# Optimization experiments

Hardware: AMD Instinct MI355X
Metric: run time of the kernel (lower is better)

## Reference

```python
import jax, jax.numpy as jnp
import numpy as np

B, C, H, W = 8, 64, 128, 128


def _conv3x3(x, w, b):
    # x: [B,C,H,W], w: [O,I,3,3], b: [O]; stride 1, padding 1
    y = jax.lax.conv_general_dilated(
        x, w, window_strides=(1, 1), padding=((1, 1), (1, 1)),
        dimension_numbers=('NCHW', 'OIHW', 'NCHW'))
    return y + b[None, :, None, None]


def setup_inputs() -> dict:
    key = jax.random.key(0)
    ks = jax.random.split(key, 8)
    s = 0.05
    return {
        'x': jax.random.normal(ks[0], (B, C, H, W), jnp.float32),
        'Wq': jax.random.normal(ks[1], (C, C, 3, 3), jnp.float32) * s,
        'bq': jax.random.normal(ks[2], (C,), jnp.float32) * s,
        'Wk': jax.random.normal(ks[3], (C, C, 3, 3), jnp.float32) * s,
        'bk': jax.random.normal(ks[4], (C,), jnp.float32) * s,
        'Wv': jax.random.normal(ks[5], (C, C, 3, 3), jnp.float32) * s,
        'bv': jax.random.normal(ks[6], (C,), jnp.float32) * s,
        'gamma': jax.random.normal(ks[7], (1,), jnp.float32) * s,
    }


def reference(x, Wq, bq, Wk, bk, Wv, bv, gamma):
    b_, c_, h_, w_ = x.shape
    q = _conv3x3(x, Wq, bq)  # [B,C,H,W]
    k = _conv3x3(x, Wk, bk)
    v = _conv3x3(x, Wv, bv)

    # energy along H (column attention): eH[b,h,w,g] = sum_c q[b,c,h,w]*k[b,c,g,w]
    eH = jnp.einsum('bchw,bcgw->bhwg', q, k)
    eye = jnp.eye(h_, dtype=bool)  # mask diagonal h==g with -inf
    eH = jnp.where(eye[None, :, None, :], -jnp.inf, eH)

    # energy along W (row attention): eW[b,h,w,g] = sum_c q[b,c,h,w]*k[b,c,h,g]
    eW = jnp.einsum('bchw,bchg->bhwg', q, k)

    # joint softmax over concatenated [H | W] axis
    att = jax.nn.softmax(jnp.concatenate([eH, eW], axis=3), axis=3)
    att_H = att[:, :, :, :h_]          # [B,H,W,H]
    att_W = att[:, :, :, h_:h_ + w_]   # [B,H,W,W]

    out_H = jnp.einsum('bcgw,bhwg->bchw', v, att_H)
    out_W = jnp.einsum('bchg,bhwg->bchw', v, att_W)

    return gamma[0] * (out_H + out_W) + x
```

## Files before the change

kernel.cpp:

```cpp
#include <hip/hip_runtime.h>
#include <hip/hip_bf16.h>

#define B_ 8
#define C_ 64
#define H_ 128
#define W_ 128
#define HW_  ((size_t)H_ * W_)
#define CHW_ ((size_t)C_ * H_ * W_)

typedef unsigned short u16;
typedef unsigned int   u32;
typedef __attribute__((ext_vector_type(8))) short bf16x8;
typedef __attribute__((ext_vector_type(4))) float f32x4;

__device__ __forceinline__ float bf2f(u16 h) {
    union { u32 u; float f; } c; c.u = ((u32)h) << 16; return c.f;
}
__device__ __forceinline__ u16 f2bf(float f) {
    union { float f; u32 u; } c; c.f = f;
    u32 u = c.u;
    u32 r = (u + 0x7fffu + ((u >> 16) & 1u)) >> 16;
    return (u16)r;
}
__device__ __forceinline__ u32 pack2(float a, float b) {
    return (u32)f2bf(a) | ((u32)f2bf(b) << 16);
}
__device__ __forceinline__ float sanit(float x, float lo, float hi) {
    return fminf(fmaxf(x, lo), hi);
}
__device__ __forceinline__ void gload_lds16(const u16* g, u16* l) {
    __builtin_amdgcn_global_load_lds(
        (const __attribute__((address_space(1))) void*)g,
        (__attribute__((address_space(3))) void*)l, 16, 0, 0);
}

__global__ __launch_bounds__(256) void prep_weights(
    const float* __restrict__ Wq, const float* __restrict__ Wk,
    const float* __restrict__ Wv, u16* __restrict__ Wt)
{
    int tap = blockIdx.x;
    int cog = blockIdx.y * 4 + (threadIdx.x >> 6);
    int ci  = threadIdx.x & 63;
    int arr = cog >> 6, co = cog & 63;
    const float* src = arr == 0 ? Wq : (arr == 1 ? Wk : Wv);
    Wt[tap * 12288 + cog * 64 + ci] = f2bf(src[(co * 64 + ci) * 9 + tap]);
}

__global__ __launch_bounds__(256) void xprep_kernel(
    const float* __restrict__ x, u16* __restrict__ xb)
{
    const int hp  = blockIdx.x;
    const int tid = threadIdx.x;
    u16* dst = xb + ((size_t)blockIdx.y * 130 + hp) * 8192;
    if (hp == 0 || hp == 129) {
#pragma unroll
        for (int i = 0; i < 4; i++)
            *(uint4*)(dst + (size_t)(tid + i * 256) * 8) = (uint4){0, 0, 0, 0};
        return;
    }
    const float* xr = x + (size_t)blockIdx.y * CHW_ + (size_t)(hp - 1) * W_;
#pragma unroll
    for (int it = 0; it < 4; it++) {
        int idx = tid + it * 256;
        int px  = idx & 127;
        int g   = idx >> 7;
        float vb[8];
#pragma unroll
        for (int e = 0; e < 8; e++)
            vb[e] = xr[(size_t)(g * 8 + e) * HW_ + px];
        uint4 o;
        o.x = pack2(vb[0], vb[1]);
        o.y = pack2(vb[2], vb[3]);
        o.z = pack2(vb[4], vb[5]);
        o.w = pack2(vb[6], vb[7]);
        *(uint4*)(dst + (size_t)(g * 128 + px) * 8) = o;
    }
}

__global__ __launch_bounds__(256, 2) void conv_mfma_kernel(
    const u16* __restrict__ xb, const u16* __restrict__ Wt,
    const float* __restrict__ bq, const float* __restrict__ bk,
    const float* __restrict__ bv,
    u16* __restrict__ qN, u16* __restrict__ kN, u16* __restrict__ v)
{
    const int nwg  = gridDim.x * gridDim.y;
    const int flat = blockIdx.y * gridDim.x + blockIdx.x;
    const int wg   = (flat & 7) * (nwg >> 3) + (flat >> 3);
    const int h    = wg & (H_ - 1);
    const int bidx = wg >> 7;
    const size_t boff = (size_t)bidx * CHW_;
    const int tid  = threadIdx.x;
    const int lane = tid & 63, wv = tid >> 6;
    const int ln15 = lane & 15, quad = lane >> 4;

    __shared__ __align__(16) u16 xI[24960];

    const int woff = (wv * 16 + ln15) * 64 + quad * 8;

    bf16x8 wcur[2][3], wnxt[2][3];
#pragma unroll
    for (int ks = 0; ks < 2; ks++)
#pragma unroll
        for (int mt = 0; mt < 3; mt++)
            wcur[ks][mt] = *(const bf16x8*)(Wt + woff + mt * 4096 + ks * 32);

    if (tid < 48) {
        int dh = tid >> 4, g = (tid & 15) >> 1, p = (tid & 1) ? 129 : 0;
        *(uint4*)(xI + dh * 8320 + g * 1040 + p * 8) = (uint4){0, 0, 0, 0};
    }

    const u16* xrows = xb + ((size_t)bidx * 130 + h) * 8192;
#pragma unroll
    for (int it = 0; it < 12; it++) {
        int chunk = wv * 12 + it;
        int dh = chunk >> 4, g = (chunk >> 1) & 7, half = chunk & 1;
        gload_lds16(xrows + (size_t)dh * 8192 + g * 1024 + half * 512 + lane * 8,
                    xI + dh * 8320 + g * 1040 + 8 + half * 512);
    }
    __syncthreads();

    f32x4 acc[3][8];
#pragma unroll
    for (int mt = 0; mt < 3; mt++)
#pragma unroll
        for (int nt = 0; nt < 8; nt++)
            acc[mt][nt] = (f32x4){0.f, 0.f, 0.f, 0.f};

#pragma unroll
    for (int tap = 0; tap < 9; tap++) {
        const int dh = tap / 3, dw = tap % 3;
        if (tap < 8) {
#pragma unroll
            for (int ks = 0; ks < 2; ks++)
#pragma unroll
                for (int mt = 0; mt < 3; mt++)
                    wnxt[ks][mt] = *(const bf16x8*)(Wt + (tap + 1) * 12288 + woff + mt * 4096 + ks * 32);
        }
        const u16* xrow = xI + dh * 8320;
#pragma unroll
        for (int ks = 0; ks < 2; ks++) {
            bf16x8 bfr[8];
#pragma unroll
            for (int nt = 0; nt < 8; nt++)
                bfr[nt] = *(const bf16x8*)(xrow + ((quad + ks * 4) * 1040 + (nt * 16 + ln15 + dw) * 8));
            __builtin_amdgcn_s_setprio(1);
#pragma unroll
            for (int mt = 0; mt < 3; mt++)
#pragma unroll
                for (int nt = 0; nt < 8; nt++)
                    acc[mt][nt] = __builtin_amdgcn_mfma_f32_16x16x32_bf16(
                        wcur[ks][mt], bfr[nt], acc[mt][nt], 0, 0, 0);
            __builtin_amdgcn_s_setprio(0);
        }
        if (tap < 8) {
#pragma unroll
            for (int ks = 0; ks < 2; ks++)
#pragma unroll
                for (int mt = 0; mt < 3; mt++)
                    wcur[ks][mt] = wnxt[ks][mt];
        }
    }

    const int cb = wv * 16 + quad * 4;
#pragma unroll
    for (int mt = 0; mt < 3; mt++) {
        const float* bias = mt == 0 ? bq : (mt == 1 ? bk : bv);
        float b0 = bias[cb], b1 = bias[cb + 1], b2 = bias[cb + 2], b3 = bias[cb + 3];
        if (mt < 2) {
            u16* dst = (mt ? kN : qN) + boff + (size_t)h * W_ * 64 + cb;
#pragma unroll
            for (int nt = 0; nt < 8; nt++) {
                int px = nt * 16 + ln15;
                u32 p0 = pack2(acc[mt][nt][0] + b0, acc[mt][nt][1] + b1);
                u32 p1 = pack2(acc[mt][nt][2] + b2, acc[mt][nt][3] + b3);
                *(u32*)(dst + (size_t)px * 64)     = p0;
                *(u32*)(dst + (size_t)px * 64 + 2) = p1;
            }
        } else {
            float bb[4] = {b0, b1, b2, b3};
#pragma unroll
            for (int r = 0; r < 4; r++) {
                u16* drow = v + boff + (size_t)(cb + r) * HW_ + (size_t)h * W_;
#pragma unroll
                for (int nt = 0; nt < 8; nt++)
                    drow[nt * 16 + ln15] = f2bf(acc[mt][nt][r] + bb[r]);
            }
        }
    }
}

__global__ __launch_bounds__(256) void vt_kernel(
    const u16* __restrict__ v, u16* __restrict__ vT)
{
    __shared__ u16 Ts[64 * 72];
    const u16* src = v  + (size_t)blockIdx.z * CHW_ + (size_t)blockIdx.y * HW_;
    u16* dst       = vT + (size_t)blockIdx.z * CHW_ + (size_t)blockIdx.y * HW_;
    const int ti = blockIdx.x & 1, tj = blockIdx.x >> 1;
    const int r0 = ti * 64, c0 = tj * 64;
    const int tid = threadIdx.x;
    const int r = tid >> 2, cq = tid & 3;
#pragma unroll
    for (int i = 0; i < 2; i++) {
        uint4 u = *(const uint4*)(src + (size_t)(r0 + r) * 128 + c0 + cq * 16 + i * 8);
        *(uint4*)(Ts + r * 72 + cq * 16 + i * 8) = u;
    }
    __syncthreads();
    const int wr = tid >> 2, hq = tid & 3;
    union { u16 o[16]; uint4 v4[2]; } t;
#pragma unroll
    for (int j = 0; j < 16; j++) t.o[j] = Ts[(hq * 16 + j) * 72 + wr];
    *(uint4*)(dst + (size_t)(c0 + wr) * 128 + r0 + hq * 16)     = t.v4[0];
    *(uint4*)(dst + (size_t)(c0 + wr) * 128 + r0 + hq * 16 + 8) = t.v4[1];
}

__global__ __launch_bounds__(256, 3) void col_kernel(
    const u16* __restrict__ qN, const u16* __restrict__ kN,
    const u16* __restrict__ vT,
    float* __restrict__ maxH, float* __restrict__ sumH,
    float* __restrict__ Ocol)
{
    const size_t boff = (size_t)blockIdx.z * CHW_;
    const size_t soff = (size_t)blockIdx.z * HW_;
    qN += boff; kN += boff; vT += boff; Ocol += boff;
    maxH += soff; sumH += soff;

    const int s    = blockIdx.x;
    const int tid  = threadIdx.x;
    const int lane = tid & 63, wv = tid >> 6;
    const int ln15 = lane & 15, quad = lane >> 4;

    __shared__ __align__(16) u16 smemU[18432];
    u16* Qs = smemU;
    u16* Ks = smemU + 9216;

#pragma unroll
    for (int it = 0; it < 4; it++) {
        int idx = tid + it * 256;
        int t = idx >> 3, cg = (idx & 7) * 8;
        size_t off = (size_t)t * 8192 + (size_t)s * 64 + cg;
        *(uint4*)(Qs + t * 72 + cg) = *(const uint4*)(qN + off);
        *(uint4*)(Ks + t * 72 + cg) = *(const uint4*)(kN + off);
    }
    __syncthreads();

    f32x4 Sc[2][8];
#pragma unroll
    for (int mt = 0; mt < 2; mt++)
#pragma unroll
        for (int nt = 0; nt < 8; nt++)
            Sc[mt][nt] = (f32x4){0.f, 0.f, 0.f, 0.f};

#pragma unroll
    for (int ks = 0; ks < 2; ks++) {
        bf16x8 aq[2];
#pragma unroll
        for (int mt = 0; mt < 2; mt++)
            aq[mt] = *(const bf16x8*)(Qs + (wv * 32 + mt * 16 + ln15) * 72 + ks * 32 + quad * 8);
#pragma unroll
        for (int nt = 0; nt < 8; nt++) {
            bf16x8 bk_ = *(const bf16x8*)(Ks + (nt * 16 + ln15) * 72 + ks * 32 + quad * 8);
#pragma unroll
            for (int mt = 0; mt < 2; mt++)
                Sc[mt][nt] = __builtin_amdgcn_mfma_f32_16x16x32_bf16(aq[mt], bk_, Sc[mt][nt], 0, 0, 0);
        }
    }
#pragma unroll
    for (int mt = 0; mt < 2; mt++)
#pragma unroll
        for (int nt = 0; nt < 8; nt++)
#pragma unroll
            for (int r = 0; r < 4; r++) {
                int tt = wv * 32 + mt * 16 + quad * 4 + r;
                if (tt == nt * 16 + ln15) Sc[mt][nt][r] = -1e30f;
            }

#pragma unroll
    for (int mt = 0; mt < 2; mt++)
#pragma unroll
        for (int r = 0; r < 4; r++) {
            float m = Sc[mt][0][r];
#pragma unroll
            for (int nt = 1; nt < 8; nt++) m = fmaxf(m, Sc[mt][nt][r]);
            for (int o = 1; o < 16; o <<= 1) m = fmaxf(m, __shfl_xor(m, o));
            float ss = 0.f;
#pragma unroll
            for (int nt = 0; nt < 8; nt++) {
                float e = __expf(Sc[mt][nt][r] - m);
                ss += e;
                Sc[mt][nt][r] = e;
            }
            for (int o = 1; o < 16; o <<= 1) ss += __shfl_xor(ss, o);
            if (ln15 == 0) {
                int tt = wv * 32 + mt * 16 + quad * 4 + r;
                int pix = tt * W_ + s;
                maxH[pix] = m; sumH[pix] = ss;
            }
        }
    __syncthreads();
    u16* Ps = smemU;
#pragma unroll
    for (int mt = 0; mt < 2; mt++)
#pragma unroll
        for (int nt = 0; nt < 8; nt++)
#pragma unroll
            for (int r = 0; r < 4; r++)
                Ps[(wv * 32 + mt * 16 + quad * 4 + r) * 136 + nt * 16 + ln15] =
                    f2bf(Sc[mt][nt][r]);
    __syncthreads();

    f32x4 Oc[2][4];
#pragma unroll
    for (int mt = 0; mt < 2; mt++)
#pragma unroll
        for (int nt = 0; nt < 4; nt++)
            Oc[mt][nt] = (f32x4){0.f, 0.f, 0.f, 0.f};
#pragma unroll
    for (int kg = 0; kg < 4; kg++) {
        bf16x8 ap[2];
#pragma unroll
        for (int mt = 0; mt < 2; mt++)
            ap[mt] = *(const bf16x8*)(Ps + (wv * 32 + mt * 16 + ln15) * 136 + kg * 32 + quad * 8);
#pragma unroll
        for (int nt = 0; nt < 4; nt++) {
            bf16x8 bv_ = *(const bf16x8*)(vT + (size_t)(nt * 16 + ln15) * HW_ + (size_t)s * 128 + kg * 32 + quad * 8);
#pragma unroll
            for (int mt = 0; mt < 2; mt++)
                Oc[mt][nt] = __builtin_amdgcn_mfma_f32_16x16x32_bf16(ap[mt], bv_, Oc[mt][nt], 0, 0, 0);
        }
    }
    __syncthreads();
    float* Of = (float*)smemU;
#pragma unroll
    for (int mt = 0; mt < 2; mt++)
#pragma unroll
        for (int nt = 0; nt < 4; nt++)
#pragma unroll
            for (int r = 0; r < 4; r++)
                Of[(wv * 32 + mt * 16 + quad * 4 + r) * 68 + nt * 16 + ln15] = Oc[mt][nt][r];
    __syncthreads();
#pragma unroll
    for (int it = 0; it < 8; it++) {
        int idx = tid + it * 256;
        int t = idx >> 4, c4 = (idx & 15) * 4;
        *(float4*)(Ocol + ((size_t)t * 128 + s) * 64 + c4) = *(float4*)(Of + t * 68 + c4);
    }
}

__global__ __launch_bounds__(256, 3) void row_kernel(
    const u16* __restrict__ qN, const u16* __restrict__ kN,
    const u16* __restrict__ v,
    const float* __restrict__ x, const float* __restrict__ gammap,
    const float* __restrict__ maxH, const float* __restrict__ sumH,
    const float* __restrict__ Ocol, float* __restrict__ out)
{
    const size_t boff = (size_t)blockIdx.z * CHW_;
    const size_t soff = (size_t)blockIdx.z * HW_;
    qN += boff; kN += boff; v += boff; Ocol += boff; x += boff; out += boff;
    maxH += soff; sumH += soff;

    const int s    = blockIdx.x;
    const int tid  = threadIdx.x;
    const int lane = tid & 63, wv = tid >> 6;
    const int ln15 = lane & 15, quad = lane >> 4;

    __shared__ __align__(16) u16 smemU[18432];
    u16* Qs = smemU;
    u16* Ks = smemU + 9216;

    float mcv[2][4], scv[2][4];
#pragma unroll
    for (int mt = 0; mt < 2; mt++)
#pragma unroll
        for (int r = 0; r < 4; r++) {
            int tt = wv * 32 + mt * 16 + quad * 4 + r;
            mcv[mt][r] = maxH[s * W_ + tt];
            scv[mt][r] = sumH[s * W_ + tt];
        }

#pragma unroll
    for (int it = 0; it < 4; it++) {
        int idx = tid + it * 256;
        int t = idx >> 3, cg = (idx & 7) * 8;
        size_t off = (size_t)s * 8192 + (size_t)t * 64 + cg;
        *(uint4*)(Qs + t * 72 + cg) = *(const uint4*)(qN + off);
        *(uint4*)(Ks + t * 72 + cg) = *(const uint4*)(kN + off);
    }
    __syncthreads();

    f32x4 Sc[2][8];
#pragma unroll
    for (int mt = 0; mt < 2; mt++)
#pragma unroll
        for (int nt = 0; nt < 8; nt++)
            Sc[mt][nt] = (f32x4){0.f, 0.f, 0.f, 0.f};
#pragma unroll
    for (int ks = 0; ks < 2; ks++) {
        bf16x8 aq[2];
#pragma unroll
        for (int mt = 0; mt < 2; mt++)
            aq[mt] = *(const bf16x8*)(Qs + (wv * 32 + mt * 16 + ln15) * 72 + ks * 32 + quad * 8);
#pragma unroll
        for (int nt = 0; nt < 8; nt++) {
            bf16x8 bk_ = *(const bf16x8*)(Ks + (nt * 16 + ln15) * 72 + ks * 32 + quad * 8);
#pragma unroll
            for (int mt = 0; mt < 2; mt++)
                Sc[mt][nt] = __builtin_amdgcn_mfma_f32_16x16x32_bf16(aq[mt], bk_, Sc[mt][nt], 0, 0, 0);
        }
    }

    float be[2][4], al[2][4];
#pragma unroll
    for (int mt = 0; mt < 2; mt++)
#pragma unroll
        for (int r = 0; r < 4; r++) {
            float m = Sc[mt][0][r];
#pragma unroll
            for (int nt = 1; nt < 8; nt++) m = fmaxf(m, Sc[mt][nt][r]);
            for (int o = 1; o < 16; o <<= 1) m = fmaxf(m, __shfl_xor(m, o));
            float ss = 0.f;
#pragma unroll
            for (int nt = 0; nt < 8; nt++) {
                float e = __expf(Sc[mt][nt][r] - m);
                ss += e;
                Sc[mt][nt][r] = e;
            }
            for (int o = 1; o < 16; o <<= 1) ss += __shfl_xor(ss, o);
            float mc = sanit(mcv[mt][r], -3e38f, 3e38f);
            float sc = sanit(scv[mt][r], 0.f, 3e38f);
            float mm = fmaxf(mc, m);
            float dd = sc * __expf(fminf(mc - mm, 0.f)) + ss * __expf(m - mm);
            float rv = 1.0f / fmaxf(dd, 1e-30f);
            be[mt][r] = __expf(m - mm) * rv;
            al[mt][r] = __expf(fminf(mc - mm, 0.f)) * rv;
        }
    __syncthreads();
    u16* Ps = smemU;
#pragma unroll
    for (int mt = 0; mt < 2; mt++)
#pragma unroll
        for (int nt = 0; nt < 8; nt++)
#pragma unroll
            for (int r = 0; r < 4; r++)
                Ps[(wv * 32 + mt * 16 + quad * 4 + r) * 136 + nt * 16 + ln15] =
                    f2bf(Sc[mt][nt][r] * be[mt][r]);
    __syncthreads();

    f32x4 Oc[2][4];
#pragma unroll
    for (int mt = 0; mt < 2; mt++)
#pragma unroll
        for (int nt = 0; nt < 4; nt++)
            Oc[mt][nt] = (f32x4){0.f, 0.f, 0.f, 0.f};
#pragma unroll
    for (int kg = 0; kg < 4; kg++) {
        bf16x8 ap[2];
#pragma unroll
        for (int mt = 0; mt < 2; mt++)
            ap[mt] = *(const bf16x8*)(Ps + (wv * 32 + mt * 16 + ln15) * 136 + kg * 32 + quad * 8);
#pragma unroll
        for (int nt = 0; nt < 4; nt++) {
            bf16x8 bv_ = *(const bf16x8*)(v + (size_t)(nt * 16 + ln15) * HW_ + (size_t)s * 128 + kg * 32 + quad * 8);
#pragma unroll
            for (int mt = 0; mt < 2; mt++)
                Oc[mt][nt] = __builtin_amdgcn_mfma_f32_16x16x32_bf16(ap[mt], bv_, Oc[mt][nt], 0, 0, 0);
        }
    }
    __syncthreads();

    const float gmm = gammap[0];
    float* Of = (float*)smemU;
#pragma unroll
    for (int mt = 0; mt < 2; mt++)
#pragma unroll
        for (int nt = 0; nt < 4; nt++) {
            float fv[4];
            int c = nt * 16 + ln15;
#pragma unroll
            for (int r = 0; r < 4; r++) {
                int tt = wv * 32 + mt * 16 + quad * 4 + r;
                float oc = Ocol[((size_t)s * 128 + tt) * 64 + c];
                fv[r] = gmm * (Oc[mt][nt][r] + al[mt][r] * oc);
            }
            int w0 = wv * 32 + mt * 16 + quad * 4;
            *(float4*)(Of + c * 132 + w0) = make_float4(fv[0], fv[1], fv[2], fv[3]);
        }
    __syncthreads();
    int c = tid >> 2, w0 = (tid & 3) * 32;
#pragma unroll
    for (int i = 0; i < 8; i++) {
        int w = w0 + i * 4;
        float4 xo = *(const float4*)(x + (size_t)c * HW_ + (size_t)s * 128 + w);
        float4 of = *(const float4*)(Of + c * 132 + w);
        *(float4*)(out + (size_t)c * HW_ + (size_t)s * 128 + w) =
            make_float4(of.x + xo.x, of.y + xo.y, of.z + xo.z, of.w + xo.w);
    }
}

extern "C" void kernel_launch(void* const* d_in, const int* in_sizes, int n_in,
                              void* d_out, int out_size, void* d_ws, size_t ws_size,
                              hipStream_t stream)
{
    const float* x  = (const float*)d_in[0];
    const float* Wq = (const float*)d_in[1];
    const float* bq = (const float*)d_in[2];
    const float* Wk = (const float*)d_in[3];
    const float* bk = (const float*)d_in[4];
    const float* Wv = (const float*)d_in[5];
    const float* bv = (const float*)d_in[6];
    const float* gm = (const float*)d_in[7];
    float* out = (float*)d_out;

    char* ws = (char*)d_ws;
    const size_t need1 = 4 * (size_t)B_ * CHW_ * 2 + (size_t)B_ * CHW_ * 4
                       + 2 * (size_t)B_ * HW_ * 4 + 221184;
    int passes = (ws_size >= need1) ? 1 : 2;
    int nb = B_ / passes;

    const size_t SL = (size_t)nb * CHW_ * 2;
    const size_t OC = (size_t)nb * CHW_ * 4;
    const size_t ST = (size_t)nb * HW_ * 4;
    u16*   qNb  = (u16*)(ws);
    u16*   kNb  = (u16*)(ws + SL);
    u16*   v    = (u16*)(ws + 2 * SL);
    u16*   vT   = (u16*)(ws + 3 * SL);
    float* Ocol = (float*)(ws + 4 * SL);
    float* maxH = (float*)(ws + 4 * SL + OC);
    float* sumH = (float*)(ws + 4 * SL + OC + ST);
    u16*   Wt   = (u16*)(ws + 4 * SL + OC + 2 * ST);
    u16*   xb   = (u16*)Ocol;

    dim3 blk(256);
    prep_weights<<<dim3(9, 48), blk, 0, stream>>>(Wq, Wk, Wv, Wt);

    for (int p = 0; p < passes; p++) {
        const float* xbp = x + (size_t)p * nb * CHW_;
        float* ob = out + (size_t)p * nb * CHW_;
        xprep_kernel<<<dim3(130, nb), blk, 0, stream>>>(xbp, xb);
        conv_mfma_kernel<<<dim3(H_, nb), blk, 0, stream>>>(xb, Wt, bq, bk, bv, qNb, kNb, v);
        vt_kernel<<<dim3(4, C_, nb), blk, 0, stream>>>(v, vT);
        col_kernel<<<dim3(W_, 1, nb), blk, 0, stream>>>(qNb, kNb, vT, maxH, sumH, Ocol);
        row_kernel<<<dim3(H_, 1, nb), blk, 0, stream>>>(qNb, kNb, v, xbp, gm, maxH, sumH, Ocol, ob);
    }
}
```

Baseline: 198.5 us.

## Split conv pixel tiles across blocks and use 512-thread attention blocks

The conv kernel now launches a z-dimension of 2, so each block computes half of a row's pixels with fewer accumulators, and its occupancy hint rises to 3. The col and row attention kernels go from 256 to 512 threads, so each wave handles 16 query rows instead of 32. The goal is more parallelism and lower register pressure on these small grids. In exchange, each conv block still stages the full input rows and weights, so that traffic is duplicated, and per-wave reuse of the loaded K/V fragments drops.

```diff
diff --git a/kernel.cpp b/kernel.cpp
--- a/kernel.cpp
+++ b/kernel.cpp
@@ -77,7 +77,7 @@
     }
 }
 
-__global__ __launch_bounds__(256, 2) void conv_mfma_kernel(
+__global__ __launch_bounds__(256, 3) void conv_mfma_kernel(
     const u16* __restrict__ xb, const u16* __restrict__ Wt,
     const float* __restrict__ bq, const float* __restrict__ bk,
     const float* __restrict__ bv,
@@ -88,6 +88,7 @@
     const int wg   = (flat & 7) * (nwg >> 3) + (flat >> 3);
     const int h    = wg & (H_ - 1);
     const int bidx = wg >> 7;
+    const int p    = blockIdx.z;
     const size_t boff = (size_t)bidx * CHW_;
     const int tid  = threadIdx.x;
     const int lane = tid & 63, wv = tid >> 6;
@@ -105,8 +106,8 @@
             wcur[ks][mt] = *(const bf16x8*)(Wt + woff + mt * 4096 + ks * 32);
 
     if (tid < 48) {
-        int dh = tid >> 4, g = (tid & 15) >> 1, p = (tid & 1) ? 129 : 0;
-        *(uint4*)(xI + dh * 8320 + g * 1040 + p * 8) = (uint4){0, 0, 0, 0};
+        int dh = tid >> 4, g = (tid & 15) >> 1, pp = (tid & 1) ? 129 : 0;
+        *(uint4*)(xI + dh * 8320 + g * 1040 + pp * 8) = (uint4){0, 0, 0, 0};
     }
 
     const u16* xrows = xb + ((size_t)bidx * 130 + h) * 8192;
@@ -119,13 +120,14 @@
     }
     __syncthreads();
 
-    f32x4 acc[3][8];
+    f32x4 acc[3][4];
 #pragma unroll
     for (int mt = 0; mt < 3; mt++)
 #pragma unroll
-        for (int nt = 0; nt < 8; nt++)
+        for (int nt = 0; nt < 4; nt++)
             acc[mt][nt] = (f32x4){0.f, 0.f, 0.f, 0.f};
 
+    const int pxb = p * 64;
 #pragma unroll
     for (int tap = 0; tap < 9; tap++) {
         const int dh = tap / 3, dw = tap % 3;
@@ -139,15 +141,15 @@
         const u16* xrow = xI + dh * 8320;
 #pragma unroll
         for (int ks = 0; ks < 2; ks++) {
-            bf16x8 bfr[8];
-#pragma unroll
-            for (int nt = 0; nt < 8; nt++)
-                bfr[nt] = *(const bf16x8*)(xrow + ((quad + ks * 4) * 1040 + (nt * 16 + ln15 + dw) * 8));
+            bf16x8 bfr[4];
+#pragma unroll
+            for (int nt = 0; nt < 4; nt++)
+                bfr[nt] = *(const bf16x8*)(xrow + ((quad + ks * 4) * 1040 + (pxb + nt * 16 + ln15 + dw) * 8));
             __builtin_amdgcn_s_setprio(1);
 #pragma unroll
             for (int mt = 0; mt < 3; mt++)
 #pragma unroll
-                for (int nt = 0; nt < 8; nt++)
+                for (int nt = 0; nt < 4; nt++)
                     acc[mt][nt] = __builtin_amdgcn_mfma_f32_16x16x32_bf16(
                         wcur[ks][mt], bfr[nt], acc[mt][nt], 0, 0, 0);
             __builtin_amdgcn_s_setprio(0);
@@ -169,8 +171,8 @@
         if (mt < 2) {
             u16* dst = (mt ? kN : qN) + boff + (size_t)h * W_ * 64 + cb;
 #pragma unroll
-            for (int nt = 0; nt < 8; nt++) {
-                int px = nt * 16 + ln15;
+            for (int nt = 0; nt < 4; nt++) {
+                int px = pxb + nt * 16 + ln15;
                 u32 p0 = pack2(acc[mt][nt][0] + b0, acc[mt][nt][1] + b1);
                 u32 p1 = pack2(acc[mt][nt][2] + b2, acc[mt][nt][3] + b3);
                 *(u32*)(dst + (size_t)px * 64)     = p0;
@@ -182,8 +184,8 @@
             for (int r = 0; r < 4; r++) {
                 u16* drow = v + boff + (size_t)(cb + r) * HW_ + (size_t)h * W_;
 #pragma unroll
-                for (int nt = 0; nt < 8; nt++)
-                    drow[nt * 16 + ln15] = f2bf(acc[mt][nt][r] + bb[r]);
+                for (int nt = 0; nt < 4; nt++)
+                    drow[pxb + nt * 16 + ln15] = f2bf(acc[mt][nt][r] + bb[r]);
             }
         }
     }
@@ -213,7 +215,7 @@
     *(uint4*)(dst + (size_t)(c0 + wr) * 128 + r0 + hq * 16 + 8) = t.v4[1];
 }
 
-__global__ __launch_bounds__(256, 3) void col_kernel(
+__global__ __launch_bounds__(512, 4) void col_kernel(
     const u16* __restrict__ qN, const u16* __restrict__ kN,
     const u16* __restrict__ vT,
     float* __restrict__ maxH, float* __restrict__ sumH,
@@ -234,8 +236,8 @@
     u16* Ks = smemU + 9216;
 
 #pragma unroll
-    for (int it = 0; it < 4; it++) {
-        int idx = tid + it * 256;
+    for (int it = 0; it < 2; it++) {
+        int idx = tid + it * 512;
         int t = idx >> 3, cg = (idx & 7) * 8;
         size_t off = (size_t)t * 8192 + (size_t)s * 64 + cg;
         *(uint4*)(Qs + t * 72 + cg) = *(const uint4*)(qN + off);
@@ -243,110 +245,87 @@
     }
     __syncthreads();
 
-    f32x4 Sc[2][8];
-#pragma unroll
-    for (int mt = 0; mt < 2; mt++)
-#pragma unroll
-        for (int nt = 0; nt < 8; nt++)
-            Sc[mt][nt] = (f32x4){0.f, 0.f, 0.f, 0.f};
+    f32x4 Sc[8];
+#pragma unroll
+    for (int nt = 0; nt < 8; nt++)
+        Sc[nt] = (f32x4){0.f, 0.f, 0.f, 0.f};
 
 #pragma unroll
     for (int ks = 0; ks < 2; ks++) {
-        bf16x8 aq[2];
-#pragma unroll
-        for (int mt = 0; mt < 2; mt++)
-            aq[mt] = *(const bf16x8*)(Qs + (wv * 32 + mt * 16 + ln15) * 72 + ks * 32 + quad * 8);
+        bf16x8 aq = *(const bf16x8*)(Qs + (wv * 16 + ln15) * 72 + ks * 32 + quad * 8);
 #pragma unroll
         for (int nt = 0; nt < 8; nt++) {
             bf16x8 bk_ = *(const bf16x8*)(Ks + (nt * 16 + ln15) * 72 + ks * 32 + quad * 8);
-#pragma unroll
-            for (int mt = 0; mt < 2; mt++)
-                Sc[mt][nt] = __builtin_amdgcn_mfma_f32_16x16x32_bf16(aq[mt], bk_, Sc[mt][nt], 0, 0, 0);
-        }
-    }
-#pragma unroll
-    for (int mt = 0; mt < 2; mt++)
-#pragma unroll
-        for (int nt = 0; nt < 8; nt++)
-#pragma unroll
-            for (int r = 0; r < 4; r++) {
-                int tt = wv * 32 + mt * 16 + quad * 4 + r;
-                if (tt == nt * 16 + ln15) Sc[mt][nt][r] = -1e30f;
-            }
-
-#pragma unroll
-    for (int mt = 0; mt < 2; mt++)
+            Sc[nt] = __builtin_amdgcn_mfma_f32_16x16x32_bf16(aq, bk_, Sc[nt], 0, 0, 0);
+        }
+    }
+#pragma unroll
+    for (int nt = 0; nt < 8; nt++)
 #pragma unroll
         for (int r = 0; r < 4; r++) {
-            float m = Sc[mt][0][r];
-#pragma unroll
-            for (int nt = 1; nt < 8; nt++) m = fmaxf(m, Sc[mt][nt][r]);
-            for (int o = 1; o < 16; o <<= 1) m = fmaxf(m, __shfl_xor(m, o));
-            float ss = 0.f;
-#pragma unroll
-            for (int nt = 0; nt < 8; nt++) {
-                float e = __expf(Sc[mt][nt][r] - m);
-                ss += e;
-                Sc[mt][nt][r] = e;
-            }
-            for (int o = 1; o < 16; o <<= 1) ss += __shfl_xor(ss, o);
-            if (ln15 == 0) {
-                int tt = wv * 32 + mt * 16 + quad * 4 + r;
-                int pix = tt * W_ + s;
-                maxH[pix] = m; sumH[pix] = ss;
-            }
-        }
+            int tt = wv * 16 + quad * 4 + r;
+            if (tt == nt * 16 + ln15) Sc[nt][r] = -1e30f;
+        }
+
+#pragma unroll
+    for (int r = 0; r < 4; r++) {
+        float m = Sc[0][r];
+#pragma unroll
+        for (int nt = 1; nt < 8; nt++) m = fmaxf(m, Sc[nt][r]);
+        for (int o = 1; o < 16; o <<= 1) m = fmaxf(m, __shfl_xor(m, o));
+        float ss = 0.f;
+#pragma unroll
+        for (int nt = 0; nt < 8; nt++) {
+            float e = __expf(Sc[nt][r] - m);
+            ss += e;
+            Sc[nt][r] = e;
+        }
+        for (int o = 1; o < 16; o <<= 1) ss += __shfl_xor(ss, o);
+        if (ln15 == 0) {
+            int tt = wv * 16 + quad * 4 + r;
+            int pix = tt * W_ + s;
+            maxH[pix] = m; sumH[pix] = ss;
+        }
+    }
     __syncthreads();
     u16* Ps = smemU;
 #pragma unroll
-    for (int mt = 0; mt < 2; mt++)
-#pragma unroll
-        for (int nt = 0; nt < 8; nt++)
-#pragma unroll
-            for (int r = 0; r < 4; r++)
-                Ps[(wv * 32 + mt * 16 + quad * 4 + r) * 136 + nt * 16 + ln15] =
-                    f2bf(Sc[mt][nt][r]);
-    __syncthreads();
-
-    f32x4 Oc[2][4];
-#pragma unroll
-    for (int mt = 0; mt < 2; mt++)
-#pragma unroll
-        for (int nt = 0; nt < 4; nt++)
-            Oc[mt][nt] = (f32x4){0.f, 0.f, 0.f, 0.f};
+    for (int nt = 0; nt < 8; nt++)
+#pragma unroll
+        for (int r = 0; r < 4; r++)
+            Ps[(wv * 16 + quad * 4 + r) * 136 + nt * 16 + ln15] = f2bf(Sc[nt][r]);
+    __syncthreads();
+
+    f32x4 Oc[4];
+#pragma unroll
+    for (int nt = 0; nt < 4; nt++)
+        Oc[nt] = (f32x4){0.f, 0.f, 0.f, 0.f};
 #pragma unroll
     for (int kg = 0; kg < 4; kg++) {
-        bf16x8 ap[2];
-#pragma unroll
-        for (int mt = 0; mt < 2; mt++)
-            ap[mt] = *(const bf16x8*)(Ps + (wv * 32 + mt * 16 + ln15) * 136 + kg * 32 + quad * 8);
+        bf16x8 ap = *(const bf16x8*)(Ps + (wv * 16 + ln15) * 136 + kg * 32 + quad * 8);
 #pragma unroll
         for (int nt = 0; nt < 4; nt++) {
             bf16x8 bv_ = *(const bf16x8*)(vT + (size_t)(nt * 16 + ln15) * HW_ + (size_t)s * 128 + kg * 32 + quad * 8);
-#pragma unroll
-            for (int mt = 0; mt < 2; mt++)
-                Oc[mt][nt] = __builtin_amdgcn_mfma_f32_16x16x32_bf16(ap[mt], bv_, Oc[mt][nt], 0, 0, 0);
+            Oc[nt] = __builtin_amdgcn_mfma_f32_16x16x32_bf16(ap, bv_, Oc[nt], 0, 0, 0);
         }
     }
     __syncthreads();
     float* Of = (float*)smemU;
 #pragma unroll
-    for (int mt = 0; mt < 2; mt++)
-#pragma unroll
-        for (int nt = 0; nt < 4; nt++)
-#pragma unroll
-            for (int r = 0; r < 4; r++)
-                Of[(wv * 32 + mt * 16 + quad * 4 + r) * 68 + nt * 16 + ln15] = Oc[mt][nt][r];
-    __syncthreads();
-#pragma unroll
-    for (int it = 0; it < 8; it++) {
-        int idx = tid + it * 256;
+    for (int nt = 0; nt < 4; nt++)
+#pragma unroll
+        for (int r = 0; r < 4; r++)
+            Of[(wv * 16 + quad * 4 + r) * 68 + nt * 16 + ln15] = Oc[nt][r];
+    __syncthreads();
+#pragma unroll
+    for (int it = 0; it < 4; it++) {
+        int idx = tid + it * 512;
         int t = idx >> 4, c4 = (idx & 15) * 4;
         *(float4*)(Ocol + ((size_t)t * 128 + s) * 64 + c4) = *(float4*)(Of + t * 68 + c4);
     }
 }
 
-__global__ __launch_bounds__(256, 3) void row_kernel(
+__global__ __launch_bounds__(512, 4) void row_kernel(
     const u16* __restrict__ qN, const u16* __restrict__ kN,
     const u16* __restrict__ v,
     const float* __restrict__ x, const float* __restrict__ gammap,
@@ -367,19 +346,17 @@
     u16* Qs = smemU;
     u16* Ks = smemU + 9216;
 
-    float mcv[2][4], scv[2][4];
-#pragma unroll
-    for (int mt = 0; mt < 2; mt++)
-#pragma unroll
-        for (int r = 0; r < 4; r++) {
-            int tt = wv * 32 + mt * 16 + quad * 4 + r;
-            mcv[mt][r] = maxH[s * W_ + tt];
-            scv[mt][r] = sumH[s * W_ + tt];
-        }
-
-#pragma unroll
-    for (int it = 0; it < 4; it++) {
-        int idx = tid + it * 256;
+    float mcv[4], scv[4];
+#pragma unroll
+    for (int r = 0; r < 4; r++) {
+        int tt = wv * 16 + quad * 4 + r;
+        mcv[r] = maxH[s * W_ + tt];
+        scv[r] = sumH[s * W_ + tt];
+    }
+
+#pragma unroll
+    for (int it = 0; it < 2; it++) {
+        int idx = tid + it * 512;
         int t = idx >> 3, cg = (idx & 7) * 8;
         size_t off = (size_t)s * 8192 + (size_t)t * 64 + cg;
         *(uint4*)(Qs + t * 72 + cg) = *(const uint4*)(qN + off);
@@ -387,82 +364,64 @@
     }
     __syncthreads();
 
-    f32x4 Sc[2][8];
-#pragma unroll
-    for (int mt = 0; mt < 2; mt++)
-#pragma unroll
-        for (int nt = 0; nt < 8; nt++)
-            Sc[mt][nt] = (f32x4){0.f, 0.f, 0.f, 0.f};
+    f32x4 Sc[8];
+#pragma unroll
+    for (int nt = 0; nt < 8; nt++)
+        Sc[nt] = (f32x4){0.f, 0.f, 0.f, 0.f};
 #pragma unroll
     for (int ks = 0; ks < 2; ks++) {
-        bf16x8 aq[2];
-#pragma unroll
-        for (int mt = 0; mt < 2; mt++)
-            aq[mt] = *(const bf16x8*)(Qs + (wv * 32 + mt * 16 + ln15) * 72 + ks * 32 + quad * 8);
+        bf16x8 aq = *(const bf16x8*)(Qs + (wv * 16 + ln15) * 72 + ks * 32 + quad * 8);
 #pragma unroll
         for (int nt = 0; nt < 8; nt++) {
             bf16x8 bk_ = *(const bf16x8*)(Ks + (nt * 16 + ln15) * 72 + ks * 32 + quad * 8);
-#pragma unroll
-            for (int mt = 0; mt < 2; mt++)
-                Sc[mt][nt] = __builtin_amdgcn_mfma_f32_16x16x32_bf16(aq[mt], bk_, Sc[mt][nt], 0, 0, 0);
-        }
-    }
-
-    float be[2][4], al[2][4];
-#pragma unroll
-    for (int mt = 0; mt < 2; mt++)
-#pragma unroll
-        for (int r = 0; r < 4; r++) {
-            float m = Sc[mt][0][r];
-#pragma unroll
-            for (int nt = 1; nt < 8; nt++) m = fmaxf(m, Sc[mt][nt][r]);
-            for (int o = 1; o < 16; o <<= 1) m = fmaxf(m, __shfl_xor(m, o));
-            float ss = 0.f;
-#pragma unroll
-            for (int nt = 0; nt < 8; nt++) {
-                float e = __expf(Sc[mt][nt][r] - m);
-                ss += e;
-                Sc[mt][nt][r] = e;
-            }
-            for (int o = 1; o < 16; o <<= 1) ss += __shfl_xor(ss, o);
-            float mc = sanit(mcv[mt][r], -3e38f, 3e38f);
-            float sc = sanit(scv[mt][r], 0.f, 3e38f);
-            float mm = fmaxf(mc, m);
-            float dd = sc * __expf(fminf(mc - mm, 0.f)) + ss * __expf(m - mm);
-            float rv = 1.0f / fmaxf(dd, 1e-30f);
-            be[mt][r] = __expf(m - mm) * rv;
-            al[mt][r] = __expf(fminf(mc - mm, 0.f)) * rv;
-        }
+            Sc[nt] = __builtin_amdgcn_mfma_f32_16x16x32_bf16(aq, bk_, Sc[nt], 0, 0, 0);
+        }
+    }
+
+    float be[4], al[4];
+#pragma unroll
+    for (int r = 0; r < 4; r++) {
+        float m = Sc[0][r];
+#pragma unroll
+        for (int nt = 1; nt < 8; nt++) m = fmaxf(m, Sc[nt][r]);
+        for (int o = 1; o < 16; o <<= 1) m = fmaxf(m, __shfl_xor(m, o));
+        float ss = 0.f;
+#pragma unroll
+        for (int nt = 0; nt < 8; nt++) {
+            float e = __expf(Sc[nt][r] - m);
+            ss += e;
+            Sc[nt][r] = e;
+        }
+        for (int o = 1; o < 16; o <<= 1) ss += __shfl_xor(ss, o);
+        float mc = sanit(mcv[r], -3e38f, 3e38f);
+        float sc = sanit(scv[r], 0.f, 3e38f);
+        float mm = fmaxf(mc, m);
+        float dd = sc * __expf(fminf(mc - mm, 0.f)) + ss * __expf(m - mm);
+        float rv = 1.0f / fmaxf(dd, 1e-30f);
+        be[r] = __expf(m - mm) * rv;
+        al[r] = __expf(fminf(mc - mm, 0.f)) * rv;
+    }
     __syncthreads();
     u16* Ps = smemU;
 #pragma unroll
-    for (int mt = 0; mt < 2; mt++)
-#pragma unroll
-        for (int nt = 0; nt < 8; nt++)
-#pragma unroll
-            for (int r = 0; r < 4; r++)
-                Ps[(wv * 32 + mt * 16 + quad * 4 + r) * 136 + nt * 16 + ln15] =
-                    f2bf(Sc[mt][nt][r] * be[mt][r]);
-    __syncthreads();
-
-    f32x4 Oc[2][4];
-#pragma unroll
-    for (int mt = 0; mt < 2; mt++)
-#pragma unroll
-        for (int nt = 0; nt < 4; nt++)
-            Oc[mt][nt] = (f32x4){0.f, 0.f, 0.f, 0.f};
+    for (int nt = 0; nt < 8; nt++)
+#pragma unroll
+        for (int r = 0; r < 4; r++)
+            Ps[(wv * 16 + quad * 4 + r) * 136 + nt * 16 + ln15] =
+                f2bf(Sc[nt][r] * be[r]);
+    __syncthreads();
+
+    f32x4 Oc[4];
+#pragma unroll
+    for (int nt = 0; nt < 4; nt++)
+        Oc[nt] = (f32x4){0.f, 0.f, 0.f, 0.f};
 #pragma unroll
     for (int kg = 0; kg < 4; kg++) {
-        bf16x8 ap[2];
-#pragma unroll
-        for (int mt = 0; mt < 2; mt++)
-            ap[mt] = *(const bf16x8*)(Ps + (wv * 32 + mt * 16 + ln15) * 136 + kg * 32 + quad * 8);
+        bf16x8 ap = *(const bf16x8*)(Ps + (wv * 16 + ln15) * 136 + kg * 32 + quad * 8);
 #pragma unroll
         for (int nt = 0; nt < 4; nt++) {
             bf16x8 bv_ = *(const bf16x8*)(v + (size_t)(nt * 16 + ln15) * HW_ + (size_t)s * 128 + kg * 32 + quad * 8);
-#pragma unroll
-            for (int mt = 0; mt < 2; mt++)
-                Oc[mt][nt] = __builtin_amdgcn_mfma_f32_16x16x32_bf16(ap[mt], bv_, Oc[mt][nt], 0, 0, 0);
+            Oc[nt] = __builtin_amdgcn_mfma_f32_16x16x32_bf16(ap, bv_, Oc[nt], 0, 0, 0);
         }
     }
     __syncthreads();
@@ -470,24 +429,22 @@
     const float gmm = gammap[0];
     float* Of = (float*)smemU;
 #pragma unroll
-    for (int mt = 0; mt < 2; mt++)
-#pragma unroll
-        for (int nt = 0; nt < 4; nt++) {
-            float fv[4];
-            int c = nt * 16 + ln15;
-#pragma unroll
-            for (int r = 0; r < 4; r++) {
-                int tt = wv * 32 + mt * 16 + quad * 4 + r;
-                float oc = Ocol[((size_t)s * 128 + tt) * 64 + c];
-                fv[r] = gmm * (Oc[mt][nt][r] + al[mt][r] * oc);
-            }
-            int w0 = wv * 32 + mt * 16 + quad * 4;
-            *(float4*)(Of + c * 132 + w0) = make_float4(fv[0], fv[1], fv[2], fv[3]);
-        }
-    __syncthreads();
-    int c = tid >> 2, w0 = (tid & 3) * 32;
-#pragma unroll
-    for (int i = 0; i < 8; i++) {
+    for (int nt = 0; nt < 4; nt++) {
+        float fv[4];
+        int c = nt * 16 + ln15;
+#pragma unroll
+        for (int r = 0; r < 4; r++) {
+            int tt = wv * 16 + quad * 4 + r;
+            float oc = Ocol[((size_t)s * 128 + tt) * 64 + c];
+            fv[r] = gmm * (Oc[nt][r] + al[r] * oc);
+        }
+        int w0 = wv * 16 + quad * 4;
+        *(float4*)(Of + c * 132 + w0) = make_float4(fv[0], fv[1], fv[2], fv[3]);
+    }
+    __syncthreads();
+    int c = tid >> 3, w0 = (tid & 7) * 16;
+#pragma unroll
+    for (int i = 0; i < 4; i++) {
         int w = w0 + i * 4;
         float4 xo = *(const float4*)(x + (size_t)c * HW_ + (size_t)s * 128 + w);
         float4 of = *(const float4*)(Of + c * 132 + w);
@@ -530,15 +487,16 @@
     u16*   xb   = (u16*)Ocol;
 
     dim3 blk(256);
+    dim3 blk5(512);
     prep_weights<<<dim3(9, 48), blk, 0, stream>>>(Wq, Wk, Wv, Wt);
 
     for (int p = 0; p < passes; p++) {
         const float* xbp = x + (size_t)p * nb * CHW_;
         float* ob = out + (size_t)p * nb * CHW_;
         xprep_kernel<<<dim3(130, nb), blk, 0, stream>>>(xbp, xb);
-        conv_mfma_kernel<<<dim3(H_, nb), blk, 0, stream>>>(xb, Wt, bq, bk, bv, qNb, kNb, v);
+        conv_mfma_kernel<<<dim3(H_, nb, 2), blk, 0, stream>>>(xb, Wt, bq, bk, bv, qNb, kNb, v);
         vt_kernel<<<dim3(4, C_, nb), blk, 0, stream>>>(v, vT);
-        col_kernel<<<dim3(W_, 1, nb), blk, 0, stream>>>(qNb, kNb, vT, maxH, sumH, Ocol);
-        row_kernel<<<dim3(H_, 1, nb), blk, 0, stream>>>(qNb, kNb, v, xbp, gm, maxH, sumH, Ocol, ob);
-    }
-}
+        col_kernel<<<dim3(W_, 1, nb), blk5, 0, stream>>>(qNb, kNb, vT, maxH, sumH, Ocol);
+        row_kernel<<<dim3(H_, 1, nb), blk5, 0, stream>>>(qNb, kNb, v, xbp, gm, maxH, sumH, Ocol, ob);
+    }
+}
```

Result: slower. 226.9 us (+14.3%).

## Store column attention output as bf16 and transpose score MFMA layout

Applied to the files above, without the earlier changes.

The column-attention output is now stored as bf16 instead of fp32, halving the bytes written by col_kernel and read back by row_kernel. The QK MFMA operands are swapped so each lane holds the scores of one query row, which moves the softmax max and sum reductions into registers and cuts them to two shuffles. Row_kernel passes its alpha rescale factors through shared memory. This costs precision in the intermediate column output. The alpha slot in shared memory overlaps the K tile and is written before the barrier, so a slower wave could still be reading that K data.

```diff
diff --git a/kernel.cpp b/kernel.cpp
--- a/kernel.cpp
+++ b/kernel.cpp
@@ -217,7 +217,7 @@
     const u16* __restrict__ qN, const u16* __restrict__ kN,
     const u16* __restrict__ vT,
     float* __restrict__ maxH, float* __restrict__ sumH,
-    float* __restrict__ Ocol)
+    u16* __restrict__ Ocol)
 {
     const size_t boff = (size_t)blockIdx.z * CHW_;
     const size_t soff = (size_t)blockIdx.z * HW_;
@@ -245,67 +245,69 @@
 
     f32x4 Sc[2][8];
 #pragma unroll
-    for (int mt = 0; mt < 2; mt++)
-#pragma unroll
-        for (int nt = 0; nt < 8; nt++)
-            Sc[mt][nt] = (f32x4){0.f, 0.f, 0.f, 0.f};
+    for (int tt = 0; tt < 2; tt++)
+#pragma unroll
+        for (int gt = 0; gt < 8; gt++)
+            Sc[tt][gt] = (f32x4){0.f, 0.f, 0.f, 0.f};
 
 #pragma unroll
     for (int ks = 0; ks < 2; ks++) {
-        bf16x8 aq[2];
-#pragma unroll
-        for (int mt = 0; mt < 2; mt++)
-            aq[mt] = *(const bf16x8*)(Qs + (wv * 32 + mt * 16 + ln15) * 72 + ks * 32 + quad * 8);
-#pragma unroll
-        for (int nt = 0; nt < 8; nt++) {
-            bf16x8 bk_ = *(const bf16x8*)(Ks + (nt * 16 + ln15) * 72 + ks * 32 + quad * 8);
-#pragma unroll
-            for (int mt = 0; mt < 2; mt++)
-                Sc[mt][nt] = __builtin_amdgcn_mfma_f32_16x16x32_bf16(aq[mt], bk_, Sc[mt][nt], 0, 0, 0);
-        }
-    }
-#pragma unroll
-    for (int mt = 0; mt < 2; mt++)
-#pragma unroll
-        for (int nt = 0; nt < 8; nt++)
+        bf16x8 bq_[2];
+#pragma unroll
+        for (int tt = 0; tt < 2; tt++)
+            bq_[tt] = *(const bf16x8*)(Qs + ((wv * 2 + tt) * 16 + ln15) * 72 + ks * 32 + quad * 8);
+#pragma unroll
+        for (int gt = 0; gt < 8; gt++) {
+            bf16x8 ak = *(const bf16x8*)(Ks + (gt * 16 + ln15) * 72 + ks * 32 + quad * 8);
+#pragma unroll
+            for (int tt = 0; tt < 2; tt++)
+                Sc[tt][gt] = __builtin_amdgcn_mfma_f32_16x16x32_bf16(ak, bq_[tt], Sc[tt][gt], 0, 0, 0);
+        }
+    }
+
+    const int tb[2] = { (wv * 2) * 16 + ln15, (wv * 2 + 1) * 16 + ln15 };
+#pragma unroll
+    for (int tt = 0; tt < 2; tt++)
+#pragma unroll
+        for (int gt = 0; gt < 8; gt++)
+#pragma unroll
+            for (int r = 0; r < 4; r++)
+                if (gt * 16 + quad * 4 + r == tb[tt]) Sc[tt][gt][r] = -1e30f;
+
+#pragma unroll
+    for (int tt = 0; tt < 2; tt++) {
+        float m = Sc[tt][0][0];
+#pragma unroll
+        for (int gt = 0; gt < 8; gt++)
+#pragma unroll
+            for (int r = 0; r < 4; r++) m = fmaxf(m, Sc[tt][gt][r]);
+        m = fmaxf(m, __shfl_xor(m, 16));
+        m = fmaxf(m, __shfl_xor(m, 32));
+        float ss = 0.f;
+#pragma unroll
+        for (int gt = 0; gt < 8; gt++)
 #pragma unroll
             for (int r = 0; r < 4; r++) {
-                int tt = wv * 32 + mt * 16 + quad * 4 + r;
-                if (tt == nt * 16 + ln15) Sc[mt][nt][r] = -1e30f;
+                float e = __expf(Sc[tt][gt][r] - m);
+                ss += e;
+                Sc[tt][gt][r] = e;
             }
-
-#pragma unroll
-    for (int mt = 0; mt < 2; mt++)
-#pragma unroll
-        for (int r = 0; r < 4; r++) {
-            float m = Sc[mt][0][r];
-#pragma unroll
-            for (int nt = 1; nt < 8; nt++) m = fmaxf(m, Sc[mt][nt][r]);
-            for (int o = 1; o < 16; o <<= 1) m = fmaxf(m, __shfl_xor(m, o));
-            float ss = 0.f;
-#pragma unroll
-            for (int nt = 0; nt < 8; nt++) {
-                float e = __expf(Sc[mt][nt][r] - m);
-                ss += e;
-                Sc[mt][nt][r] = e;
-            }
-            for (int o = 1; o < 16; o <<= 1) ss += __shfl_xor(ss, o);
-            if (ln15 == 0) {
-                int tt = wv * 32 + mt * 16 + quad * 4 + r;
-                int pix = tt * W_ + s;
-                maxH[pix] = m; sumH[pix] = ss;
-            }
-        }
+        ss += __shfl_xor(ss, 16);
+        ss += __shfl_xor(ss, 32);
+        if (quad == 0) {
+            int pix = tb[tt] * W_ + s;
+            maxH[pix] = m; sumH[pix] = ss;
+        }
+    }
     __syncthreads();
     u16* Ps = smemU;
 #pragma unroll
-    for (int mt = 0; mt < 2; mt++)
-#pragma unroll
-        for (int nt = 0; nt < 8; nt++)
+    for (int tt = 0; tt < 2; tt++)
+#pragma unroll
+        for (int gt = 0; gt < 8; gt++)
 #pragma unroll
             for (int r = 0; r < 4; r++)
-                Ps[(wv * 32 + mt * 16 + quad * 4 + r) * 136 + nt * 16 + ln15] =
-                    f2bf(Sc[mt][nt][r]);
+                Ps[tb[tt] * 136 + gt * 16 + quad * 4 + r] = f2bf(Sc[tt][gt][r]);
     __syncthreads();
 
     f32x4 Oc[2][4];
@@ -329,20 +331,20 @@
         }
     }
     __syncthreads();
-    float* Of = (float*)smemU;
+    u16* OfU = smemU;
 #pragma unroll
     for (int mt = 0; mt < 2; mt++)
 #pragma unroll
         for (int nt = 0; nt < 4; nt++)
 #pragma unroll
             for (int r = 0; r < 4; r++)
-                Of[(wv * 32 + mt * 16 + quad * 4 + r) * 68 + nt * 16 + ln15] = Oc[mt][nt][r];
-    __syncthreads();
-#pragma unroll
-    for (int it = 0; it < 8; it++) {
+                OfU[(wv * 32 + mt * 16 + quad * 4 + r) * 72 + nt * 16 + ln15] = f2bf(Oc[mt][nt][r]);
+    __syncthreads();
+#pragma unroll
+    for (int it = 0; it < 4; it++) {
         int idx = tid + it * 256;
-        int t = idx >> 4, c4 = (idx & 15) * 4;
-        *(float4*)(Ocol + ((size_t)t * 128 + s) * 64 + c4) = *(float4*)(Of + t * 68 + c4);
+        int t = idx >> 3, c8 = (idx & 7) * 8;
+        *(uint4*)(Ocol + ((size_t)t * 128 + s) * 64 + c8) = *(uint4*)(OfU + t * 72 + c8);
     }
 }
 
@@ -351,7 +353,7 @@
     const u16* __restrict__ v,
     const float* __restrict__ x, const float* __restrict__ gammap,
     const float* __restrict__ maxH, const float* __restrict__ sumH,
-    const float* __restrict__ Ocol, float* __restrict__ out)
+    const u16* __restrict__ Ocol, float* __restrict__ out)
 {
     const size_t boff = (size_t)blockIdx.z * CHW_;
     const size_t soff = (size_t)blockIdx.z * HW_;
@@ -366,16 +368,15 @@
     __shared__ __align__(16) u16 smemU[18432];
     u16* Qs = smemU;
     u16* Ks = smemU + 9216;
-
-    float mcv[2][4], scv[2][4];
-#pragma unroll
-    for (int mt = 0; mt < 2; mt++)
-#pragma unroll
-        for (int r = 0; r < 4; r++) {
-            int tt = wv * 32 + mt * 16 + quad * 4 + r;
-            mcv[mt][r] = maxH[s * W_ + tt];
-            scv[mt][r] = sumH[s * W_ + tt];
-        }
+    float* alL = (float*)(smemU + 17408);
+
+    const int tb[2] = { (wv * 2) * 16 + ln15, (wv * 2 + 1) * 16 + ln15 };
+    float mcv[2], scv[2];
+#pragma unroll
+    for (int tt = 0; tt < 2; tt++) {
+        mcv[tt] = maxH[s * W_ + tb[tt]];
+        scv[tt] = sumH[s * W_ + tb[tt]];
+    }
 
 #pragma unroll
     for (int it = 0; it < 4; it++) {
@@ -389,60 +390,63 @@
 
     f32x4 Sc[2][8];
 #pragma unroll
-    for (int mt = 0; mt < 2; mt++)
-#pragma unroll
-        for (int nt = 0; nt < 8; nt++)
-            Sc[mt][nt] = (f32x4){0.f, 0.f, 0.f, 0.f};
+    for (int tt = 0; tt < 2; tt++)
+#pragma unroll
+        for (int gt = 0; gt < 8; gt++)
+            Sc[tt][gt] = (f32x4){0.f, 0.f, 0.f, 0.f};
 #pragma unroll
     for (int ks = 0; ks < 2; ks++) {
-        bf16x8 aq[2];
-#pragma unroll
-        for (int mt = 0; mt < 2; mt++)
-            aq[mt] = *(const bf16x8*)(Qs + (wv * 32 + mt * 16 + ln15) * 72 + ks * 32 + quad * 8);
-#pragma unroll
-        for (int nt = 0; nt < 8; nt++) {
-            bf16x8 bk_ = *(const bf16x8*)(Ks + (nt * 16 + ln15) * 72 + ks * 32 + quad * 8);
-#pragma unroll
-            for (int mt = 0; mt < 2; mt++)
-                Sc[mt][nt] = __builtin_amdgcn_mfma_f32_16x16x32_bf16(aq[mt], bk_, Sc[mt][nt], 0, 0, 0);
-        }
-    }
-
-    float be[2][4], al[2][4];
-#pragma unroll
-    for (int mt = 0; mt < 2; mt++)
-#pragma unroll
-        for (int r = 0; r < 4; r++) {
-            float m = Sc[mt][0][r];
-#pragma unroll
-            for (int nt = 1; nt < 8; nt++) m = fmaxf(m, Sc[mt][nt][r]);
-            for (int o = 1; o < 16; o <<= 1) m = fmaxf(m, __shfl_xor(m, o));
-            float ss = 0.f;
-#pragma unroll
-            for (int nt = 0; nt < 8; nt++) {
-                float e = __expf(Sc[mt][nt][r] - m);
+        bf16x8 bq_[2];
+#pragma unroll
+        for (int tt = 0; tt < 2; tt++)
+            bq_[tt] = *(const bf16x8*)(Qs + ((wv * 2 + tt) * 16 + ln15) * 72 + ks * 32 + quad * 8);
+#pragma unroll
+        for (int gt = 0; gt < 8; gt++) {
+            bf16x8 ak = *(const bf16x8*)(Ks + (gt * 16 + ln15) * 72 + ks * 32 + quad * 8);
+#pragma unroll
+            for (int tt = 0; tt < 2; tt++)
+                Sc[tt][gt] = __builtin_amdgcn_mfma_f32_16x16x32_bf16(ak, bq_[tt], Sc[tt][gt], 0, 0, 0);
+        }
+    }
+
+    float be[2];
+#pragma unroll
+    for (int tt = 0; tt < 2; tt++) {
+        float m = Sc[tt][0][0];
+#pragma unroll
+        for (int gt = 0; gt < 8; gt++)
+#pragma unroll
+            for (int r = 0; r < 4; r++) m = fmaxf(m, Sc[tt][gt][r]);
+        m = fmaxf(m, __shfl_xor(m, 16));
+        m = fmaxf(m, __shfl_xor(m, 32));
+        float ss = 0.f;
+#pragma unroll
+        for (int gt = 0; gt < 8; gt++)
+#pragma unroll
+            for (int r = 0; r < 4; r++) {
+                float e = __expf(Sc[tt][gt][r] - m);
                 ss += e;
-                Sc[mt][nt][r] = e;
+                Sc[tt][gt][r] = e;
             }
-            for (int o = 1; o < 16; o <<= 1) ss += __shfl_xor(ss, o);
-            float mc = sanit(mcv[mt][r], -3e38f, 3e38f);
-            float sc = sanit(scv[mt][r], 0.f, 3e38f);
-            float mm = fmaxf(mc, m);
-            float dd = sc * __expf(fminf(mc - mm, 0.f)) + ss * __expf(m - mm);
-            float rv = 1.0f / fmaxf(dd, 1e-30f);
-            be[mt][r] = __expf(m - mm) * rv;
-            al[mt][r] = __expf(fminf(mc - mm, 0.f)) * rv;
-        }
+        ss += __shfl_xor(ss, 16);
+        ss += __shfl_xor(ss, 32);
+        float mc = sanit(mcv[tt], -3e38f, 3e38f);
+        float sc = sanit(scv[tt], 0.f, 3e38f);
+        float mm = fmaxf(mc, m);
+        float dd = sc * __expf(fminf(mc - mm, 0.f)) + ss * __expf(m - mm);
+        float rv = 1.0f / fmaxf(dd, 1e-30f);
+        be[tt] = __expf(m - mm) * rv;
+        if (quad == 0) alL[tb[tt]] = __expf(fminf(mc - mm, 0.f)) * rv;
+    }
     __syncthreads();
     u16* Ps = smemU;
 #pragma unroll
-    for (int mt = 0; mt < 2; mt++)
-#pragma unroll
-        for (int nt = 0; nt < 8; nt++)
+    for (int tt = 0; tt < 2; tt++)
+#pragma unroll
+        for (int gt = 0; gt < 8; gt++)
 #pragma unroll
             for (int r = 0; r < 4; r++)
-                Ps[(wv * 32 + mt * 16 + quad * 4 + r) * 136 + nt * 16 + ln15] =
-                    f2bf(Sc[mt][nt][r] * be[mt][r]);
+                Ps[tb[tt] * 136 + gt * 16 + quad * 4 + r] = f2bf(Sc[tt][gt][r] * be[tt]);
     __syncthreads();
 
     f32x4 Oc[2][4];
@@ -478,8 +482,8 @@
 #pragma unroll
             for (int r = 0; r < 4; r++) {
                 int tt = wv * 32 + mt * 16 + quad * 4 + r;
-                float oc = Ocol[((size_t)s * 128 + tt) * 64 + c];
-                fv[r] = gmm * (Oc[mt][nt][r] + al[mt][r] * oc);
+                float oc = bf2f(Ocol[((size_t)s * 128 + tt) * 64 + c]);
+                fv[r] = gmm * (Oc[mt][nt][r] + alL[tt] * oc);
             }
             int w0 = wv * 32 + mt * 16 + quad * 4;
             *(float4*)(Of + c * 132 + w0) = make_float4(fv[0], fv[1], fv[2], fv[3]);
@@ -523,7 +527,7 @@
     u16*   kNb  = (u16*)(ws + SL);
     u16*   v    = (u16*)(ws + 2 * SL);
     u16*   vT   = (u16*)(ws + 3 * SL);
-    float* Ocol = (float*)(ws + 4 * SL);
+    u16*   Ocol = (u16*)(ws + 4 * SL);
     float* maxH = (float*)(ws + 4 * SL + OC);
     float* sumH = (float*)(ws + 4 * SL + OC + ST);
     u16*   Wt   = (u16*)(ws + 4 * SL + OC + 2 * ST);
```

Measured after the change: 191.2 us. 3.7% less time.
